# Optimization experiments

Measured on AMD Instinct MI355X. Metric: run time of the kernel, lower is better.

The kernel has to match this reference:

```python
import jax, jax.numpy as jnp
import numpy as np
from jax.ops import segment_sum

N_GRAPHS, N_PER = 100, 1000
N = N_GRAPHS * N_PER
DEG = 32
E = N * DEG
RATIO = 0.8
K = int(np.ceil(RATIO * N_PER))  # 800, equal-size graphs -> fixed k
F_IN, F_MID, F_OUT = 128, 16, 256


def setup_inputs() -> dict:
    key = jax.random.key(0)
    ks = jax.random.split(key, 10)
    x = jax.random.normal(ks[0], (N, F_IN), dtype=jnp.float32)
    # intra-graph random edges
    epg = E // N_GRAPHS
    src_l = jax.random.randint(ks[1], (N_GRAPHS, epg), 0, N_PER)
    dst_l = jax.random.randint(ks[2], (N_GRAPHS, epg), 0, N_PER)
    offs = (jnp.arange(N_GRAPHS) * N_PER)[:, None]
    edge_index = jnp.stack([(src_l + offs).reshape(-1), (dst_l + offs).reshape(-1)]).astype(jnp.int32)
    batch = jnp.repeat(jnp.arange(N_GRAPHS, dtype=jnp.int32), N_PER)
    s = lambda fan: 1.0 / np.sqrt(fan)
    W1 = jax.random.normal(ks[3], (F_IN, F_MID), dtype=jnp.float32) * s(F_IN)
    b1 = jnp.zeros((F_MID,), dtype=jnp.float32)
    w_rel = jax.random.normal(ks[4], (F_MID, 1), dtype=jnp.float32) * s(F_MID)
    b_rel = jnp.zeros((1,), dtype=jnp.float32)
    w_root = jax.random.normal(ks[5], (F_MID, 1), dtype=jnp.float32) * s(F_MID)
    W2 = jax.random.normal(ks[6], (F_MID, F_OUT), dtype=jnp.float32) * s(F_MID)
    b2 = jnp.zeros((F_OUT,), dtype=jnp.float32)
    return {"x": x, "edge_index": edge_index, "batch": batch,
            "W1": W1, "b1": b1, "w_rel": w_rel, "b_rel": b_rel,
            "w_root": w_root, "W2": W2, "b2": b2}


def _gcn(x, src, dst, W, b, self_w, ew, n):
    # GCNConv with self-loops: D^{-1/2}(A+I)D^{-1/2} X W + b; masked variant
    deg = segment_sum(ew, dst, num_segments=n) + self_w
    dis = jnp.where(deg > 0, jax.lax.rsqrt(deg), 0.0)
    xw = x @ W
    coef = ew * dis[src] * dis[dst]                       # [E]
    agg = segment_sum(xw[src] * coef[:, None], dst, num_segments=n)
    agg = agg + xw * (self_w * dis * dis)[:, None]        # self-loop term
    return agg + b


def reference(x, edge_index, batch, W1, b1, w_rel, b_rel, w_root, W2, b2):
    src, dst = edge_index[0], edge_index[1]
    ones_n = jnp.ones((N,), dtype=x.dtype)
    ones_e = jnp.ones((src.shape[0],), dtype=x.dtype)
    # conv1 + relu
    h = jax.nn.relu(_gcn(x, src, dst, W1, b1, ones_n, ones_e, N))
    # SAGPooling score: GraphConv(16,1) -> tanh
    agg = segment_sum(h[src], dst, num_segments=N)
    score = jnp.tanh((agg @ w_rel + h @ w_root + b_rel)[:, 0])  # [N]
    # per-graph top-k (equal graph sizes -> fixed K), expressed as node mask
    sc2 = score.reshape(N_GRAPHS, N_PER)
    _, idx = jax.lax.top_k(sc2, K)
    mask = jnp.zeros((N_GRAPHS, N_PER), dtype=x.dtype)
    mask = mask.at[jnp.arange(N_GRAPHS)[:, None], idx].set(1.0).reshape(-1)  # [N]
    h = h * (score * mask)[:, None]                       # x[perm] * score[perm]
    em = mask[src] * mask[dst]                            # filter_adj as edge mask
    # conv2 + relu on surviving nodes only
    h2 = jax.nn.relu(_gcn(h, src, dst, W2, b2, mask, em, N)) * mask[:, None]
    # global mean pool over surviving nodes per graph
    sums = segment_sum(h2, batch, num_segments=N_GRAPHS)
    cnt = segment_sum(mask, batch, num_segments=N_GRAPHS)
    return sums / cnt[:, None]
```

## Files before the change

### kernel.cpp

```cpp
#include <hip/hip_runtime.h>
#include <math.h>

#define N_NODES 100000
#define NG 100
#define N_PER 1000
#define N_EDGES 3200000
#define EPG 32000
#define EPG4 8000
#define EPGP 35008
#define K_TOP 800
#define F_IN 128
#define F_MID 16
#define F_OUT 256
#define SENT 1000

typedef __attribute__((ext_vector_type(8))) short short8;
typedef __attribute__((ext_vector_type(4))) float floatx4;

__device__ __forceinline__ unsigned short f2bf(float x) {
    union { float f; unsigned int u; } c; c.f = x;
    unsigned int u = c.u;
    u = u + 0x7FFF + ((u >> 16) & 1);
    return (unsigned short)(u >> 16);
}
__device__ __forceinline__ void add4(float4& a, const float4 b) {
    a.x += b.x; a.y += b.y; a.z += b.z; a.w += b.w;
}
__device__ __forceinline__ void fma4(float4& a, const float4 b, float w) {
    a.x = fmaf(b.x, w, a.x); a.y = fmaf(b.y, w, a.y);
    a.z = fmaf(b.z, w, a.z); a.w = fmaf(b.w, w, a.w);
}

__global__ __launch_bounds__(256) void k_front(const float* __restrict__ x,
    const float* __restrict__ W1, const int* __restrict__ ei,
    unsigned short* __restrict__ csr, int* __restrict__ cntG, int* __restrict__ rsG,
    float* __restrict__ dis1G, float* __restrict__ xw1)
{
    __shared__ __align__(16) char smem[16640];
    int b = blockIdx.x, t = threadIdx.x;
    if (b < NG) {
        int g = b;
        int* cnts = (int*)smem;
        int* rs   = (int*)(smem + 4000);
        int* cur  = (int*)(smem + 8000);
        int* sums = (int*)(smem + 12000);
        for (int i = t; i < N_PER; i += 256) { cnts[i] = 0; cur[i] = 0; }
        __syncthreads();
        int ebase = g * EPG, nbase = g * N_PER;
        const int4* dst4 = (const int4*)(ei + N_EDGES + ebase);
        const int4* src4 = (const int4*)(ei + ebase);
        for (int i = t; i < EPG4; i += 256) {
            int4 d = dst4[i];
            atomicAdd(&cnts[d.x - nbase], 1);
            atomicAdd(&cnts[d.y - nbase], 1);
            atomicAdd(&cnts[d.z - nbase], 1);
            atomicAdd(&cnts[d.w - nbase], 1);
        }
        __syncthreads();
        int c[4], cpd[4], pl[4], tot;
        if (t < 250) {
            for (int r = 0; r < 4; r++) { c[r] = cnts[4 * t + r]; cpd[r] = (c[r] + 3) & ~3; }
        } else {
            for (int r = 0; r < 4; r++) { c[r] = 0; cpd[r] = 0; }
        }
        pl[0] = 0;
        for (int r = 1; r < 4; r++) pl[r] = pl[r - 1] + cpd[r - 1];
        tot = pl[3] + cpd[3];
        sums[t] = tot;
        __syncthreads();
        for (int dd = 1; dd < 256; dd <<= 1) {
            int v = (t >= dd) ? sums[t - dd] : 0;
            __syncthreads();
            sums[t] += v;
            __syncthreads();
        }
        int exc = sums[t] - tot;
        unsigned short* cg = csr + (size_t)g * EPGP;
        if (t < 250) {
            for (int r = 0; r < 4; r++) {
                int n = 4 * t + r, base = exc + pl[r];
                rs[n] = base;
                rsG[nbase + n] = base;
                cntG[nbase + n] = c[r];
                dis1G[nbase + n] = rsqrtf((float)c[r] + 1.0f);
                for (int q = c[r]; q < cpd[r]; q++) cg[base + q] = (unsigned short)SENT;
            }
        }
        __syncthreads();
        for (int i = t; i < EPG4; i += 256) {
            int4 s4 = src4[i]; int4 d4 = dst4[i];
            int dl, p;
            dl = d4.x - nbase; p = rs[dl] + atomicAdd(&cur[dl], 1); cg[p] = (unsigned short)(s4.x - nbase);
            dl = d4.y - nbase; p = rs[dl] + atomicAdd(&cur[dl], 1); cg[p] = (unsigned short)(s4.y - nbase);
            dl = d4.z - nbase; p = rs[dl] + atomicAdd(&cur[dl], 1); cg[p] = (unsigned short)(s4.z - nbase);
            dl = d4.w - nbase; p = rs[dl] + atomicAdd(&cur[dl], 1); cg[p] = (unsigned short)(s4.w - nbase);
        }
    } else {
        int tile = b - NG, n0 = tile * 16;
        float* xs = (float*)smem;
        float* ws = (float*)(smem + 8448);
        const float* xp = x + (size_t)n0 * F_IN;
        for (int i = t; i < 16 * F_IN; i += 256) {
            int n = i >> 7, k = i & 127;
            xs[n * 132 + k] = xp[i];
        }
        for (int i = t; i < F_IN * F_MID; i += 256) ws[i] = W1[i];
        __syncthreads();
        int node = t >> 4, j = t & 15;
        const float* xr = xs + node * 132;
        float acc = 0.f;
#pragma unroll 16
        for (int k = 0; k < F_IN; k++) acc += xr[k] * ws[k * F_MID + j];
        xw1[(size_t)(n0 + node) * F_MID + j] = acc;
    }
}

__global__ __launch_bounds__(1024) void k_mega(const unsigned short* __restrict__ csr,
    const int* __restrict__ cntG, const int* __restrict__ rsG,
    const float* __restrict__ dis1G, const float* __restrict__ xw1,
    const float* __restrict__ b1, const float* __restrict__ w_rel,
    const float* __restrict__ b_rel, const float* __restrict__ w_root,
    const float* __restrict__ W2, const float* __restrict__ b2,
    float* __restrict__ out)
{
    __shared__ __align__(16) float feat[(N_PER + 1) * F_MID];
    __shared__ __align__(16) unsigned short fbf[N_PER * F_MID];
    __shared__ __align__(16) unsigned short w2t[F_OUT * F_MID];
    __shared__ float sc[N_PER];
    __shared__ float msk[N_PER + 1];
    __shared__ float wsrc[N_PER + 1];
    __shared__ float dis2a[N_PER];
    __shared__ float dis1l[N_PER];
    __shared__ int   cntl[N_PER];
    __shared__ int   rsl[N_PER];
    __shared__ float ssrt[1024];
    __shared__ int cnt_gt;

    int t = threadIdx.x, g = blockIdx.x;
    int nbase = g * N_PER;
    const unsigned short* cg = csr + (size_t)g * EPGP;

    if (t < N_PER) { cntl[t] = cntG[nbase + t]; rsl[t] = rsG[nbase + t]; dis1l[t] = dis1G[nbase + t]; }
    if (t == 0) cnt_gt = 0;
    for (int i = t; i < F_OUT * F_MID; i += 1024) {
        int f = i >> 4, jj = i & 15;
        w2t[i] = f2bf(W2[jj * F_OUT + f]);
    }
    __syncthreads();

    {
        const float4* xs = (const float4*)(xw1 + (size_t)nbase * F_MID);
        float4* fd = (float4*)feat;
        for (int i = t; i < N_PER * 4; i += 1024) {
            float4 v = xs[i];
            float d = dis1l[i >> 2];
            v.x *= d; v.y *= d; v.z *= d; v.w *= d;
            fd[i] = v;
        }
        if (t < 4) { float4 z = {0.f, 0.f, 0.f, 0.f}; fd[N_PER * 4 + t] = z; }
    }
    __syncthreads();

    int grp = t >> 2, l = t & 3;
    float4 b14 = *(const float4*)(b1 + 4 * l);
    float4 wr4 = *(const float4*)(w_rel + 4 * l);
    float4 wo4 = *(const float4*)(w_root + 4 * l);
    float brel = b_rel[0];

    float4 hreg[4];
#pragma unroll
    for (int rr = 0; rr < 4; rr++) {
        int n = grp + 256 * rr;
        if (n < N_PER) {
            int c4 = (cntl[n] + 3) & ~3;
            const unsigned short* cp = cg + rsl[n];
            float4 a0 = {0,0,0,0}, a1 = a0, a2 = a0, a3 = a0;
            for (int k = 0; k < c4; k += 4) {
                uint2 wv = *(const uint2*)(cp + k);
                int s0 = wv.x & 0xFFFF, s1 = wv.x >> 16, s2 = wv.y & 0xFFFF, s3 = wv.y >> 16;
                add4(a0, *(const float4*)(feat + s0 * F_MID + 4 * l));
                add4(a1, *(const float4*)(feat + s1 * F_MID + 4 * l));
                add4(a2, *(const float4*)(feat + s2 * F_MID + 4 * l));
                add4(a3, *(const float4*)(feat + s3 * F_MID + 4 * l));
            }
            add4(a0, a1); add4(a2, a3); add4(a0, a2);
            float4 sf = *(const float4*)(feat + n * F_MID + 4 * l);
            float di = dis1l[n];
            float4 hv;
            hv.x = fmaxf(fmaf(di, a0.x + sf.x, b14.x), 0.f);
            hv.y = fmaxf(fmaf(di, a0.y + sf.y, b14.y), 0.f);
            hv.z = fmaxf(fmaf(di, a0.z + sf.z, b14.z), 0.f);
            hv.w = fmaxf(fmaf(di, a0.w + sf.w, b14.w), 0.f);
            hreg[rr] = hv;
        }
    }
    __syncthreads();
#pragma unroll
    for (int rr = 0; rr < 4; rr++) {
        int n = grp + 256 * rr;
        if (n < N_PER) *(float4*)(feat + n * F_MID + 4 * l) = hreg[rr];
    }
    __syncthreads();

#pragma unroll
    for (int rr = 0; rr < 4; rr++) {
        int n = grp + 256 * rr;
        if (n < N_PER) {
            int c4 = (cntl[n] + 3) & ~3;
            const unsigned short* cp = cg + rsl[n];
            float4 a0 = {0,0,0,0}, a1 = a0, a2 = a0, a3 = a0;
            for (int k = 0; k < c4; k += 4) {
                uint2 wv = *(const uint2*)(cp + k);
                int s0 = wv.x & 0xFFFF, s1 = wv.x >> 16, s2 = wv.y & 0xFFFF, s3 = wv.y >> 16;
                add4(a0, *(const float4*)(feat + s0 * F_MID + 4 * l));
                add4(a1, *(const float4*)(feat + s1 * F_MID + 4 * l));
                add4(a2, *(const float4*)(feat + s2 * F_MID + 4 * l));
                add4(a3, *(const float4*)(feat + s3 * F_MID + 4 * l));
            }
            add4(a0, a1); add4(a2, a3); add4(a0, a2);
            float4 sf = *(const float4*)(feat + n * F_MID + 4 * l);
            float val = a0.x * wr4.x + a0.y * wr4.y + a0.z * wr4.z + a0.w * wr4.w
                      + sf.x * wo4.x + sf.y * wo4.y + sf.z * wo4.z + sf.w * wo4.w;
            val += __shfl_xor(val, 1);
            val += __shfl_xor(val, 2);
            if (l == 0) sc[n] = tanhf(val + brel);
        }
    }
    __syncthreads();

    ssrt[t] = (t < N_PER) ? sc[t] : -1e30f;
    __syncthreads();
    for (int k2 = 2; k2 <= 1024; k2 <<= 1) {
        for (int j2 = k2 >> 1; j2 > 0; j2 >>= 1) {
            if (j2 >= 32) __syncthreads();
            int ixj = t ^ j2;
            if (ixj > t) {
                float a = ssrt[t], b = ssrt[ixj];
                bool asc = ((t & k2) == 0);
                if ((a > b) == asc) { ssrt[t] = b; ssrt[ixj] = a; }
            }
        }
    }
    __syncthreads();

    float thr = ssrt[1024 - K_TOP];
    bool pred = (t < N_PER) && (sc[t] > thr);
    unsigned long long bal = __ballot(pred);
    if ((t & 63) == 0) atomicAdd(&cnt_gt, (int)__popcll(bal));
    __syncthreads();
    int need = K_TOP - cnt_gt;
    if (t < N_PER) {
        float v = sc[t];
        float mm;
        if (v > thr) mm = 1.f;
        else if (v < thr) mm = 0.f;
        else {
            int r = 0;
            for (int q = 0; q < t; q++) if (sc[q] == thr) r++;
            mm = (r < need) ? 1.f : 0.f;
        }
        msk[t] = mm;
    }
    if (t == N_PER) { msk[SENT] = 0.f; wsrc[SENT] = 0.f; }
    __syncthreads();

#pragma unroll
    for (int rr = 0; rr < 4; rr++) {
        int n = grp + 256 * rr;
        if (n < N_PER) {
            int c4 = (cntl[n] + 3) & ~3;
            const unsigned short* cp = cg + rsl[n];
            float sm = 0.f;
            for (int k = 0; k < c4; k += 4) {
                uint2 wv = *(const uint2*)(cp + k);
                int s = (l == 0) ? (int)(wv.x & 0xFFFF) : (l == 1) ? (int)(wv.x >> 16)
                      : (l == 2) ? (int)(wv.y & 0xFFFF) : (int)(wv.y >> 16);
                sm += msk[s];
            }
            sm += __shfl_xor(sm, 1);
            sm += __shfl_xor(sm, 2);
            if (l == 0) {
                float d2 = msk[n] * (sm + 1.f);
                float di = (d2 > 0.f) ? rsqrtf(d2) : 0.f;
                dis2a[n] = di;
                wsrc[n] = sc[n] * msk[n] * di;
            }
        }
    }
    __syncthreads();

    float4 preg[4];
#pragma unroll
    for (int rr = 0; rr < 4; rr++) {
        int n = grp + 256 * rr;
        if (n < N_PER) {
            float di = dis2a[n];
            float4 pv = {0,0,0,0};
            if (di != 0.f) {
                int c4 = (cntl[n] + 3) & ~3;
                const unsigned short* cp = cg + rsl[n];
                float4 a0 = {0,0,0,0}, a1 = a0, a2 = a0, a3 = a0;
                for (int k = 0; k < c4; k += 4) {
                    uint2 wv = *(const uint2*)(cp + k);
                    int s0 = wv.x & 0xFFFF, s1 = wv.x >> 16, s2 = wv.y & 0xFFFF, s3 = wv.y >> 16;
                    float ww0 = wsrc[s0], ww1 = wsrc[s1], ww2 = wsrc[s2], ww3 = wsrc[s3];
                    fma4(a0, *(const float4*)(feat + s0 * F_MID + 4 * l), ww0);
                    fma4(a1, *(const float4*)(feat + s1 * F_MID + 4 * l), ww1);
                    fma4(a2, *(const float4*)(feat + s2 * F_MID + 4 * l), ww2);
                    fma4(a3, *(const float4*)(feat + s3 * F_MID + 4 * l), ww3);
                }
                add4(a0, a1); add4(a2, a3); add4(a0, a2);
                float4 sf = *(const float4*)(feat + n * F_MID + 4 * l);
                float wn = wsrc[n];
                pv.x = di * fmaf(sf.x, wn, a0.x);
                pv.y = di * fmaf(sf.y, wn, a0.y);
                pv.z = di * fmaf(sf.z, wn, a0.z);
                pv.w = di * fmaf(sf.w, wn, a0.w);
            }
            preg[rr] = pv;
        }
    }
    __syncthreads();
#pragma unroll
    for (int rr = 0; rr < 4; rr++) {
        int n = grp + 256 * rr;
        if (n < N_PER) *(float4*)(feat + n * F_MID + 4 * l) = preg[rr];
    }
    __syncthreads();

    for (int i = t; i < N_PER * F_MID / 2; i += 1024) {
        float2 v = *(const float2*)(feat + 2 * i);
        unsigned int pk = (unsigned int)f2bf(v.x) | ((unsigned int)f2bf(v.y) << 16);
        ((unsigned int*)fbf)[i] = pk;
    }
    __syncthreads();

    {
        int wave = t >> 6, lane = t & 63;
        int q = lane >> 4, fl = lane & 15;
        int fglob = wave * 16 + fl;
        float b2f = b2[fglob];
        short8 bfrag = {0, 0, 0, 0, 0, 0, 0, 0};
        if (q < 2) bfrag = *(const short8*)(w2t + fglob * F_MID + q * 8);
        floatx4 zero = {0.f, 0.f, 0.f, 0.f};
        float acc = 0.f;
        for (int tile = 0; tile < 63; tile++) {
            short8 afrag = {0, 0, 0, 0, 0, 0, 0, 0};
            int na = tile * 16 + fl;
            if (q < 2 && na < N_PER)
                afrag = *(const short8*)(fbf + na * F_MID + q * 8);
            floatx4 d = __builtin_amdgcn_mfma_f32_16x16x32_bf16(afrag, bfrag, zero, 0, 0, 0);
#pragma unroll
            for (int r = 0; r < 4; r++) {
                int nd = tile * 16 + q * 4 + r;
                if (nd < N_PER) acc += msk[nd] * fmaxf(d[r] + b2f, 0.f);
            }
        }
        acc += __shfl_xor(acc, 16);
        acc += __shfl_xor(acc, 32);
        if (lane < 16) out[g * F_OUT + fglob] = acc * (1.0f / (float)K_TOP);
    }
}

extern "C" void kernel_launch(void* const* d_in, const int* in_sizes, int n_in,
                              void* d_out, int out_size, void* d_ws, size_t ws_size,
                              hipStream_t stream) {
    const float* x      = (const float*)d_in[0];
    const int*   ei     = (const int*)d_in[1];
    const float* W1     = (const float*)d_in[3];
    const float* b1     = (const float*)d_in[4];
    const float* w_rel  = (const float*)d_in[5];
    const float* b_rel  = (const float*)d_in[6];
    const float* w_root = (const float*)d_in[7];
    const float* W2     = (const float*)d_in[8];
    const float* b2     = (const float*)d_in[9];
    float* out = (float*)d_out;

    char* ws = (char*)d_ws;
    size_t o = 0;
    unsigned short* csr = (unsigned short*)(ws + o); o += (size_t)NG * EPGP * sizeof(unsigned short);
    int*   cntG  = (int*)(ws + o);   o += (size_t)N_NODES * sizeof(int);
    int*   rsG   = (int*)(ws + o);   o += (size_t)N_NODES * sizeof(int);
    float* dis1G = (float*)(ws + o); o += (size_t)N_NODES * sizeof(float);
    float* xw1   = (float*)(ws + o); o += (size_t)N_NODES * F_MID * sizeof(float);

    k_front<<<NG + N_NODES / 16, 256, 0, stream>>>(x, W1, ei, csr, cntG, rsG, dis1G, xw1);
    k_mega<<<NG, 1024, 0, stream>>>(csr, cntG, rsG, dis1G, xw1,
                                    b1, w_rel, b_rel, w_root, W2, b2, out);
}
```

Baseline: 243.8 us.

## Replace bitonic top-k with radix select and project scores before aggregation

Several changes land together. The SAGPooling score now projects h onto w_rel and w_root per node first and aggregates a scalar per edge instead of 16-wide vectors. The 1024-element bitonic sort for the top-k threshold becomes a two-pass 10-bit radix histogram select. Feature rows in LDS get an XOR-style swizzle to reduce bank conflicts, conv2 pre-scales features by wsrc so the edge loop is plain adds, and the final MFMA pass splits nodes across two halves with two column tiles per wave. k_front moves to 1024-thread blocks that hold edges in registers and run a 64-node GEMM tile. This adds code complexity and more block-level syncs in the radix scans.

```diff
diff --git a/kernel.cpp b/kernel.cpp
--- a/kernel.cpp
+++ b/kernel.cpp
@@ -26,92 +26,86 @@
 __device__ __forceinline__ void add4(float4& a, const float4 b) {
     a.x += b.x; a.y += b.y; a.z += b.z; a.w += b.w;
 }
-__device__ __forceinline__ void fma4(float4& a, const float4 b, float w) {
-    a.x = fmaf(b.x, w, a.x); a.y = fmaf(b.y, w, a.y);
-    a.z = fmaf(b.z, w, a.z); a.w = fmaf(b.w, w, a.w);
-}
-
-__global__ __launch_bounds__(256) void k_front(const float* __restrict__ x,
+__device__ __forceinline__ int fidx4(int s, int l) {
+    return s * 16 + ((4 * (l + ((s >> 1) & 3))) & 15);
+}
+__device__ __forceinline__ unsigned int fkey(float f) {
+    unsigned int u = __float_as_uint(f);
+    return (u & 0x80000000u) ? ~u : (u | 0x80000000u);
+}
+
+__global__ __launch_bounds__(1024) void k_front(const float* __restrict__ x,
     const float* __restrict__ W1, const int* __restrict__ ei,
     unsigned short* __restrict__ csr, int* __restrict__ cntG, int* __restrict__ rsG,
     float* __restrict__ dis1G, float* __restrict__ xw1)
 {
-    __shared__ __align__(16) char smem[16640];
     int b = blockIdx.x, t = threadIdx.x;
     if (b < NG) {
-        int g = b;
-        int* cnts = (int*)smem;
-        int* rs   = (int*)(smem + 4000);
-        int* cur  = (int*)(smem + 8000);
-        int* sums = (int*)(smem + 12000);
-        for (int i = t; i < N_PER; i += 256) { cnts[i] = 0; cur[i] = 0; }
-        __syncthreads();
-        int ebase = g * EPG, nbase = g * N_PER;
+        __shared__ int cnts[N_PER];
+        __shared__ int cur[N_PER];
+        __shared__ int rs[N_PER];
+        __shared__ int scan[1024];
+        int g = b, ebase = g * EPG, nbase = g * N_PER;
         const int4* dst4 = (const int4*)(ei + N_EDGES + ebase);
         const int4* src4 = (const int4*)(ei + ebase);
-        for (int i = t; i < EPG4; i += 256) {
-            int4 d = dst4[i];
-            atomicAdd(&cnts[d.x - nbase], 1);
-            atomicAdd(&cnts[d.y - nbase], 1);
-            atomicAdd(&cnts[d.z - nbase], 1);
-            atomicAdd(&cnts[d.w - nbase], 1);
-        }
-        __syncthreads();
-        int c[4], cpd[4], pl[4], tot;
-        if (t < 250) {
-            for (int r = 0; r < 4; r++) { c[r] = cnts[4 * t + r]; cpd[r] = (c[r] + 3) & ~3; }
-        } else {
-            for (int r = 0; r < 4; r++) { c[r] = 0; cpd[r] = 0; }
-        }
-        pl[0] = 0;
-        for (int r = 1; r < 4; r++) pl[r] = pl[r - 1] + cpd[r - 1];
-        tot = pl[3] + cpd[3];
-        sums[t] = tot;
-        __syncthreads();
-        for (int dd = 1; dd < 256; dd <<= 1) {
-            int v = (t >= dd) ? sums[t - dd] : 0;
+        int4 dreg[8], sreg[8];
+        int ni = 0;
+        for (int i = t; i < EPG4; i += 1024) { dreg[ni] = dst4[i]; sreg[ni] = src4[i]; ni++; }
+        if (t < N_PER) { cnts[t] = 0; cur[t] = 0; }
+        __syncthreads();
+        for (int i = 0; i < ni; i++) {
+            atomicAdd(&cnts[dreg[i].x - nbase], 1);
+            atomicAdd(&cnts[dreg[i].y - nbase], 1);
+            atomicAdd(&cnts[dreg[i].z - nbase], 1);
+            atomicAdd(&cnts[dreg[i].w - nbase], 1);
+        }
+        __syncthreads();
+        int c = (t < N_PER) ? cnts[t] : 0;
+        int c4 = (c + 3) & ~3;
+        scan[t] = c4;
+        __syncthreads();
+        for (int dd = 1; dd < 1024; dd <<= 1) {
+            int v = (t >= dd) ? scan[t - dd] : 0;
             __syncthreads();
-            sums[t] += v;
+            scan[t] += v;
             __syncthreads();
         }
-        int exc = sums[t] - tot;
+        int exc = scan[t] - c4;
         unsigned short* cg = csr + (size_t)g * EPGP;
-        if (t < 250) {
-            for (int r = 0; r < 4; r++) {
-                int n = 4 * t + r, base = exc + pl[r];
-                rs[n] = base;
-                rsG[nbase + n] = base;
-                cntG[nbase + n] = c[r];
-                dis1G[nbase + n] = rsqrtf((float)c[r] + 1.0f);
-                for (int q = c[r]; q < cpd[r]; q++) cg[base + q] = (unsigned short)SENT;
-            }
-        }
-        __syncthreads();
-        for (int i = t; i < EPG4; i += 256) {
-            int4 s4 = src4[i]; int4 d4 = dst4[i];
+        if (t < N_PER) {
+            rs[t] = exc; rsG[nbase + t] = exc; cntG[nbase + t] = c;
+            dis1G[nbase + t] = rsqrtf((float)c + 1.0f);
+            for (int q = c; q < c4; q++) cg[exc + q] = (unsigned short)SENT;
+        }
+        __syncthreads();
+        for (int i = 0; i < ni; i++) {
             int dl, p;
-            dl = d4.x - nbase; p = rs[dl] + atomicAdd(&cur[dl], 1); cg[p] = (unsigned short)(s4.x - nbase);
-            dl = d4.y - nbase; p = rs[dl] + atomicAdd(&cur[dl], 1); cg[p] = (unsigned short)(s4.y - nbase);
-            dl = d4.z - nbase; p = rs[dl] + atomicAdd(&cur[dl], 1); cg[p] = (unsigned short)(s4.z - nbase);
-            dl = d4.w - nbase; p = rs[dl] + atomicAdd(&cur[dl], 1); cg[p] = (unsigned short)(s4.w - nbase);
+            dl = dreg[i].x - nbase; p = rs[dl] + atomicAdd(&cur[dl], 1); cg[p] = (unsigned short)(sreg[i].x - nbase);
+            dl = dreg[i].y - nbase; p = rs[dl] + atomicAdd(&cur[dl], 1); cg[p] = (unsigned short)(sreg[i].y - nbase);
+            dl = dreg[i].z - nbase; p = rs[dl] + atomicAdd(&cur[dl], 1); cg[p] = (unsigned short)(sreg[i].z - nbase);
+            dl = dreg[i].w - nbase; p = rs[dl] + atomicAdd(&cur[dl], 1); cg[p] = (unsigned short)(sreg[i].w - nbase);
         }
     } else {
-        int tile = b - NG, n0 = tile * 16;
-        float* xs = (float*)smem;
-        float* ws = (float*)(smem + 8448);
-        const float* xp = x + (size_t)n0 * F_IN;
-        for (int i = t; i < 16 * F_IN; i += 256) {
+        __shared__ float xs[64 * 132];
+        __shared__ float wsm[F_IN * F_MID];
+        long tile = b - NG;
+        long n0 = tile * 64;
+        int nmax = (int)((N_NODES - n0 < 64) ? (N_NODES - n0) : 64);
+        const float* xp = x + n0 * F_IN;
+        for (int i = t; i < nmax * F_IN; i += 1024) {
             int n = i >> 7, k = i & 127;
             xs[n * 132 + k] = xp[i];
         }
-        for (int i = t; i < F_IN * F_MID; i += 256) ws[i] = W1[i];
+        for (int i = t; i < F_IN * F_MID; i += 1024) wsm[i] = W1[i];
         __syncthreads();
         int node = t >> 4, j = t & 15;
-        const float* xr = xs + node * 132;
-        float acc = 0.f;
+        if (node < nmax) {
+            const float* xr = xs + node * 132;
+            float acc = 0.f;
 #pragma unroll 16
-        for (int k = 0; k < F_IN; k++) acc += xr[k] * ws[k * F_MID + j];
-        xw1[(size_t)(n0 + node) * F_MID + j] = acc;
+            for (int k = 0; k < F_IN; k++) acc += xr[k] * wsm[k * F_MID + j];
+            xw1[(n0 + node) * F_MID + j] = acc;
+        }
     }
 }
 
@@ -129,19 +123,24 @@
     __shared__ float sc[N_PER];
     __shared__ float msk[N_PER + 1];
     __shared__ float wsrc[N_PER + 1];
+    __shared__ float hw[N_PER + 1];
+    __shared__ float hro[N_PER];
     __shared__ float dis2a[N_PER];
     __shared__ float dis1l[N_PER];
-    __shared__ int   cntl[N_PER];
-    __shared__ int   rsl[N_PER];
-    __shared__ float ssrt[1024];
-    __shared__ int cnt_gt;
+    __shared__ int cntl[N_PER];
+    __shared__ int rsl[N_PER];
+    __shared__ int hist[1024];
+    __shared__ float partial[F_OUT];
+    __shared__ int sh_b1, sh_r1, sh_b2, sh_r2, sh_len, sh_cntgt;
+    __shared__ float sh_thr;
 
     int t = threadIdx.x, g = blockIdx.x;
     int nbase = g * N_PER;
     const unsigned short* cg = csr + (size_t)g * EPGP;
+    int grp = t >> 2, l = t & 3;
 
     if (t < N_PER) { cntl[t] = cntG[nbase + t]; rsl[t] = rsG[nbase + t]; dis1l[t] = dis1G[nbase + t]; }
-    if (t == 0) cnt_gt = 0;
+    if (t == 0) { sh_cntgt = 0; sh_len = 0; }
     for (int i = t; i < F_OUT * F_MID; i += 1024) {
         int f = i >> 4, jj = i & 15;
         w2t[i] = f2bf(W2[jj * F_OUT + f]);
@@ -149,19 +148,18 @@
     __syncthreads();
 
     {
-        const float4* xs = (const float4*)(xw1 + (size_t)nbase * F_MID);
-        float4* fd = (float4*)feat;
+        const float4* xsrc = (const float4*)(xw1 + (size_t)nbase * F_MID);
         for (int i = t; i < N_PER * 4; i += 1024) {
-            float4 v = xs[i];
-            float d = dis1l[i >> 2];
+            int n = i >> 2, q = i & 3;
+            float4 v = xsrc[i];
+            float d = dis1l[n];
             v.x *= d; v.y *= d; v.z *= d; v.w *= d;
-            fd[i] = v;
-        }
-        if (t < 4) { float4 z = {0.f, 0.f, 0.f, 0.f}; fd[N_PER * 4 + t] = z; }
-    }
-    __syncthreads();
-
-    int grp = t >> 2, l = t & 3;
+            *(float4*)(feat + fidx4(n, q)) = v;
+        }
+        if (t < 4) { float4 z = {0.f, 0.f, 0.f, 0.f}; *(float4*)(feat + fidx4(SENT, t)) = z; }
+    }
+    __syncthreads();
+
     float4 b14 = *(const float4*)(b1 + 4 * l);
     float4 wr4 = *(const float4*)(w_rel + 4 * l);
     float4 wo4 = *(const float4*)(w_root + 4 * l);
@@ -178,13 +176,13 @@
             for (int k = 0; k < c4; k += 4) {
                 uint2 wv = *(const uint2*)(cp + k);
                 int s0 = wv.x & 0xFFFF, s1 = wv.x >> 16, s2 = wv.y & 0xFFFF, s3 = wv.y >> 16;
-                add4(a0, *(const float4*)(feat + s0 * F_MID + 4 * l));
-                add4(a1, *(const float4*)(feat + s1 * F_MID + 4 * l));
-                add4(a2, *(const float4*)(feat + s2 * F_MID + 4 * l));
-                add4(a3, *(const float4*)(feat + s3 * F_MID + 4 * l));
+                add4(a0, *(const float4*)(feat + fidx4(s0, l)));
+                add4(a1, *(const float4*)(feat + fidx4(s1, l)));
+                add4(a2, *(const float4*)(feat + fidx4(s2, l)));
+                add4(a3, *(const float4*)(feat + fidx4(s3, l)));
             }
             add4(a0, a1); add4(a2, a3); add4(a0, a2);
-            float4 sf = *(const float4*)(feat + n * F_MID + 4 * l);
+            float4 sf = *(const float4*)(feat + fidx4(n, l));
             float di = dis1l[n];
             float4 hv;
             hv.x = fmaxf(fmaf(di, a0.x + sf.x, b14.x), 0.f);
@@ -198,8 +196,23 @@
 #pragma unroll
     for (int rr = 0; rr < 4; rr++) {
         int n = grp + 256 * rr;
-        if (n < N_PER) *(float4*)(feat + n * F_MID + 4 * l) = hreg[rr];
-    }
+        if (n < N_PER) *(float4*)(feat + fidx4(n, l)) = hreg[rr];
+    }
+    __syncthreads();
+
+#pragma unroll
+    for (int rr = 0; rr < 4; rr++) {
+        int n = grp + 256 * rr;
+        if (n < N_PER) {
+            float4 hv = *(const float4*)(feat + fidx4(n, l));
+            float p1 = hv.x * wr4.x + hv.y * wr4.y + hv.z * wr4.z + hv.w * wr4.w;
+            float p2 = hv.x * wo4.x + hv.y * wo4.y + hv.z * wo4.z + hv.w * wo4.w;
+            p1 += __shfl_xor(p1, 1); p1 += __shfl_xor(p1, 2);
+            p2 += __shfl_xor(p2, 1); p2 += __shfl_xor(p2, 2);
+            if (l == 0) { hw[n] = p1; hro[n] = p2; }
+        }
+    }
+    if (t == 0) hw[SENT] = 0.f;
     __syncthreads();
 
 #pragma unroll
@@ -208,60 +221,96 @@
         if (n < N_PER) {
             int c4 = (cntl[n] + 3) & ~3;
             const unsigned short* cp = cg + rsl[n];
-            float4 a0 = {0,0,0,0}, a1 = a0, a2 = a0, a3 = a0;
+            float sm = 0.f;
             for (int k = 0; k < c4; k += 4) {
                 uint2 wv = *(const uint2*)(cp + k);
-                int s0 = wv.x & 0xFFFF, s1 = wv.x >> 16, s2 = wv.y & 0xFFFF, s3 = wv.y >> 16;
-                add4(a0, *(const float4*)(feat + s0 * F_MID + 4 * l));
-                add4(a1, *(const float4*)(feat + s1 * F_MID + 4 * l));
-                add4(a2, *(const float4*)(feat + s2 * F_MID + 4 * l));
-                add4(a3, *(const float4*)(feat + s3 * F_MID + 4 * l));
-            }
-            add4(a0, a1); add4(a2, a3); add4(a0, a2);
-            float4 sf = *(const float4*)(feat + n * F_MID + 4 * l);
-            float val = a0.x * wr4.x + a0.y * wr4.y + a0.z * wr4.z + a0.w * wr4.w
-                      + sf.x * wo4.x + sf.y * wo4.y + sf.z * wo4.z + sf.w * wo4.w;
-            val += __shfl_xor(val, 1);
-            val += __shfl_xor(val, 2);
-            if (l == 0) sc[n] = tanhf(val + brel);
-        }
-    }
-    __syncthreads();
-
-    ssrt[t] = (t < N_PER) ? sc[t] : -1e30f;
-    __syncthreads();
-    for (int k2 = 2; k2 <= 1024; k2 <<= 1) {
-        for (int j2 = k2 >> 1; j2 > 0; j2 >>= 1) {
-            if (j2 >= 32) __syncthreads();
-            int ixj = t ^ j2;
-            if (ixj > t) {
-                float a = ssrt[t], b = ssrt[ixj];
-                bool asc = ((t & k2) == 0);
-                if ((a > b) == asc) { ssrt[t] = b; ssrt[ixj] = a; }
-            }
-        }
-    }
-    __syncthreads();
-
-    float thr = ssrt[1024 - K_TOP];
-    bool pred = (t < N_PER) && (sc[t] > thr);
-    unsigned long long bal = __ballot(pred);
-    if ((t & 63) == 0) atomicAdd(&cnt_gt, (int)__popcll(bal));
-    __syncthreads();
-    int need = K_TOP - cnt_gt;
-    if (t < N_PER) {
-        float v = sc[t];
-        float mm;
-        if (v > thr) mm = 1.f;
-        else if (v < thr) mm = 0.f;
-        else {
-            int r = 0;
-            for (int q = 0; q < t; q++) if (sc[q] == thr) r++;
-            mm = (r < need) ? 1.f : 0.f;
-        }
-        msk[t] = mm;
-    }
-    if (t == N_PER) { msk[SENT] = 0.f; wsrc[SENT] = 0.f; }
+                int s = (l == 0) ? (int)(wv.x & 0xFFFF) : (l == 1) ? (int)(wv.x >> 16)
+                      : (l == 2) ? (int)(wv.y & 0xFFFF) : (int)(wv.y >> 16);
+                sm += hw[s];
+            }
+            sm += __shfl_xor(sm, 1); sm += __shfl_xor(sm, 2);
+            if (l == 0) sc[n] = tanhf(sm + hro[n] + brel);
+        }
+    }
+    __syncthreads();
+
+    unsigned int mykey = (t < N_PER) ? fkey(sc[t]) : 0u;
+    hist[t] = 0;
+    __syncthreads();
+    if (t < N_PER) atomicAdd(&hist[mykey >> 22], 1);
+    __syncthreads();
+    {
+        int v0 = hist[t]; __syncthreads();
+        hist[1023 - t] = v0; __syncthreads();
+        for (int dd = 1; dd < 1024; dd <<= 1) {
+            int v = (t >= dd) ? hist[t - dd] : 0;
+            __syncthreads(); hist[t] += v; __syncthreads();
+        }
+        int Sb = hist[1023 - t];
+        int Snext = (t == 1023) ? 0 : hist[1022 - t];
+        if (Sb >= K_TOP && Snext < K_TOP) { sh_b1 = t; sh_r1 = K_TOP - Snext; }
+    }
+    __syncthreads();
+    int b1v = sh_b1, r1 = sh_r1;
+    hist[t] = 0;
+    __syncthreads();
+    if (t < N_PER && (int)(mykey >> 22) == b1v) atomicAdd(&hist[(mykey >> 12) & 1023], 1);
+    __syncthreads();
+    {
+        int v0 = hist[t]; __syncthreads();
+        hist[1023 - t] = v0; __syncthreads();
+        for (int dd = 1; dd < 1024; dd <<= 1) {
+            int v = (t >= dd) ? hist[t - dd] : 0;
+            __syncthreads(); hist[t] += v; __syncthreads();
+        }
+        int Sb = hist[1023 - t];
+        int Snext = (t == 1023) ? 0 : hist[1022 - t];
+        if (Sb >= r1 && Snext < r1) { sh_b2 = t; sh_r2 = r1 - Snext; }
+    }
+    __syncthreads();
+    unsigned int pref = ((unsigned int)b1v << 10) | (unsigned int)sh_b2;
+    int r2 = sh_r2;
+    __syncthreads();
+    if (t < N_PER && (mykey >> 12) == pref) { int p = atomicAdd(&sh_len, 1); hist[p] = (int)mykey; }
+    __syncthreads();
+    {
+        int L = sh_len;
+        if (t < L) {
+            unsigned int k0 = (unsigned int)hist[t];
+            int gcnt = 0, ecnt = 0;
+            for (int q2 = 0; q2 < L; q2++) {
+                unsigned int kq = (unsigned int)hist[q2];
+                gcnt += (kq > k0); ecnt += (kq == k0);
+            }
+            if (gcnt < r2 && r2 <= gcnt + ecnt)
+                sh_thr = __uint_as_float((k0 & 0x80000000u) ? (k0 & 0x7FFFFFFFu) : ~k0);
+        }
+    }
+    __syncthreads();
+    float thr = sh_thr;
+
+    {
+        bool pred = (t < N_PER) && (sc[t] > thr);
+        unsigned long long bal = __ballot(pred);
+        if ((t & 63) == 0) atomicAdd(&sh_cntgt, (int)__popcll(bal));
+    }
+    __syncthreads();
+    {
+        int need = K_TOP - sh_cntgt;
+        if (t < N_PER) {
+            float v = sc[t];
+            float mm;
+            if (v > thr) mm = 1.f;
+            else if (v < thr) mm = 0.f;
+            else {
+                int r = 0;
+                for (int q2 = 0; q2 < t; q2++) if (sc[q2] == thr) r++;
+                mm = (r < need) ? 1.f : 0.f;
+            }
+            msk[t] = mm;
+        }
+        if (t == 0) { msk[SENT] = 0.f; wsrc[SENT] = 0.f; }
+    }
     __syncthreads();
 
 #pragma unroll
@@ -277,8 +326,7 @@
                       : (l == 2) ? (int)(wv.y & 0xFFFF) : (int)(wv.y >> 16);
                 sm += msk[s];
             }
-            sm += __shfl_xor(sm, 1);
-            sm += __shfl_xor(sm, 2);
+            sm += __shfl_xor(sm, 1); sm += __shfl_xor(sm, 2);
             if (l == 0) {
                 float d2 = msk[n] * (sm + 1.f);
                 float di = (d2 > 0.f) ? rsqrtf(d2) : 0.f;
@@ -286,6 +334,16 @@
                 wsrc[n] = sc[n] * msk[n] * di;
             }
         }
+    }
+    __syncthreads();
+
+    for (int i = t; i < N_PER * 4; i += 1024) {
+        int n = i >> 2, q = i & 3;
+        float w = wsrc[n];
+        float4* p = (float4*)(feat + fidx4(n, q));
+        float4 v = *p;
+        v.x *= w; v.y *= w; v.z *= w; v.w *= w;
+        *p = v;
     }
     __syncthreads();
 
@@ -303,19 +361,17 @@
                 for (int k = 0; k < c4; k += 4) {
                     uint2 wv = *(const uint2*)(cp + k);
                     int s0 = wv.x & 0xFFFF, s1 = wv.x >> 16, s2 = wv.y & 0xFFFF, s3 = wv.y >> 16;
-                    float ww0 = wsrc[s0], ww1 = wsrc[s1], ww2 = wsrc[s2], ww3 = wsrc[s3];
-                    fma4(a0, *(const float4*)(feat + s0 * F_MID + 4 * l), ww0);
-                    fma4(a1, *(const float4*)(feat + s1 * F_MID + 4 * l), ww1);
-                    fma4(a2, *(const float4*)(feat + s2 * F_MID + 4 * l), ww2);
-                    fma4(a3, *(const float4*)(feat + s3 * F_MID + 4 * l), ww3);
+                    add4(a0, *(const float4*)(feat + fidx4(s0, l)));
+                    add4(a1, *(const float4*)(feat + fidx4(s1, l)));
+                    add4(a2, *(const float4*)(feat + fidx4(s2, l)));
+                    add4(a3, *(const float4*)(feat + fidx4(s3, l)));
                 }
                 add4(a0, a1); add4(a2, a3); add4(a0, a2);
-                float4 sf = *(const float4*)(feat + n * F_MID + 4 * l);
-                float wn = wsrc[n];
-                pv.x = di * fmaf(sf.x, wn, a0.x);
-                pv.y = di * fmaf(sf.y, wn, a0.y);
-                pv.z = di * fmaf(sf.z, wn, a0.z);
-                pv.w = di * fmaf(sf.w, wn, a0.w);
+                float4 sf = *(const float4*)(feat + fidx4(n, l));
+                pv.x = di * (a0.x + sf.x);
+                pv.y = di * (a0.y + sf.y);
+                pv.z = di * (a0.z + sf.z);
+                pv.w = di * (a0.w + sf.w);
             }
             preg[rr] = pv;
         }
@@ -324,12 +380,14 @@
 #pragma unroll
     for (int rr = 0; rr < 4; rr++) {
         int n = grp + 256 * rr;
-        if (n < N_PER) *(float4*)(feat + n * F_MID + 4 * l) = preg[rr];
-    }
-    __syncthreads();
-
-    for (int i = t; i < N_PER * F_MID / 2; i += 1024) {
-        float2 v = *(const float2*)(feat + 2 * i);
+        if (n < N_PER) *(float4*)(feat + fidx4(n, l)) = preg[rr];
+    }
+    __syncthreads();
+
+    for (int i = t; i < N_PER * 8; i += 1024) {
+        int n = i >> 3, cp2 = (i & 7) * 2;
+        int phys = n * 16 + ((cp2 + 4 * ((n >> 1) & 3)) & 15);
+        float2 v = *(const float2*)(feat + phys);
         unsigned int pk = (unsigned int)f2bf(v.x) | ((unsigned int)f2bf(v.y) << 16);
         ((unsigned int*)fbf)[i] = pk;
     }
@@ -338,27 +396,42 @@
     {
         int wave = t >> 6, lane = t & 63;
         int q = lane >> 4, fl = lane & 15;
-        int fglob = wave * 16 + fl;
-        float b2f = b2[fglob];
-        short8 bfrag = {0, 0, 0, 0, 0, 0, 0, 0};
-        if (q < 2) bfrag = *(const short8*)(w2t + fglob * F_MID + q * 8);
+        int half = wave >> 3, wcol = wave & 7;
+        int c0 = 32 * wcol + fl, c1 = c0 + 16;
+        float b2f0 = b2[c0], b2f1 = b2[c1];
+        short8 bfrag0 = {0,0,0,0,0,0,0,0}, bfrag1 = bfrag0;
+        if (q < 2) {
+            bfrag0 = *(const short8*)(w2t + c0 * F_MID + q * 8);
+            bfrag1 = *(const short8*)(w2t + c1 * F_MID + q * 8);
+        }
         floatx4 zero = {0.f, 0.f, 0.f, 0.f};
-        float acc = 0.f;
-        for (int tile = 0; tile < 63; tile++) {
-            short8 afrag = {0, 0, 0, 0, 0, 0, 0, 0};
+        float acc0 = 0.f, acc1 = 0.f;
+        int t0 = half ? 32 : 0, t1 = half ? 63 : 32;
+        for (int tile = t0; tile < t1; tile++) {
+            short8 afrag = {0,0,0,0,0,0,0,0};
             int na = tile * 16 + fl;
             if (q < 2 && na < N_PER)
                 afrag = *(const short8*)(fbf + na * F_MID + q * 8);
-            floatx4 d = __builtin_amdgcn_mfma_f32_16x16x32_bf16(afrag, bfrag, zero, 0, 0, 0);
+            floatx4 d0 = __builtin_amdgcn_mfma_f32_16x16x32_bf16(afrag, bfrag0, zero, 0, 0, 0);
+            floatx4 d1 = __builtin_amdgcn_mfma_f32_16x16x32_bf16(afrag, bfrag1, zero, 0, 0, 0);
 #pragma unroll
             for (int r = 0; r < 4; r++) {
                 int nd = tile * 16 + q * 4 + r;
-                if (nd < N_PER) acc += msk[nd] * fmaxf(d[r] + b2f, 0.f);
-            }
-        }
-        acc += __shfl_xor(acc, 16);
-        acc += __shfl_xor(acc, 32);
-        if (lane < 16) out[g * F_OUT + fglob] = acc * (1.0f / (float)K_TOP);
+                if (nd < N_PER) {
+                    float m = msk[nd];
+                    acc0 += m * fmaxf(d0[r] + b2f0, 0.f);
+                    acc1 += m * fmaxf(d1[r] + b2f1, 0.f);
+                }
+            }
+        }
+        acc0 += __shfl_xor(acc0, 16); acc0 += __shfl_xor(acc0, 32);
+        acc1 += __shfl_xor(acc1, 16); acc1 += __shfl_xor(acc1, 32);
+        if (half == 0 && lane < 16) { partial[c0] = acc0; partial[c1] = acc1; }
+        __syncthreads();
+        if (half == 1 && lane < 16) {
+            out[g * F_OUT + c0] = (partial[c0] + acc0) * (1.0f / (float)K_TOP);
+            out[g * F_OUT + c1] = (partial[c1] + acc1) * (1.0f / (float)K_TOP);
+        }
     }
 }
 
@@ -384,7 +457,8 @@
     float* dis1G = (float*)(ws + o); o += (size_t)N_NODES * sizeof(float);
     float* xw1   = (float*)(ws + o); o += (size_t)N_NODES * F_MID * sizeof(float);
 
-    k_front<<<NG + N_NODES / 16, 256, 0, stream>>>(x, W1, ei, csr, cntG, rsG, dis1G, xw1);
+    int gemm_blocks = (N_NODES + 63) / 64;
+    k_front<<<NG + gemm_blocks, 1024, 0, stream>>>(x, W1, ei, csr, cntG, rsG, dis1G, xw1);
     k_mega<<<NG, 1024, 0, stream>>>(csr, cntG, rsG, dis1G, xw1,
                                     b1, w_rel, b_rel, w_root, W2, b2, out);
 }
```

New measurement: 240.7 us. No clear change (-1.3%).
